# Kernel optimization log

Measured on AMD Instinct MI355X. Metric: run time of the kernel, lower is better.

Reference implementation:

```python
import jax, jax.numpy as jnp
import numpy as np

BN_EPS = 1e-5

def _conv1x1(h, w, b):
    # h: [N, Cin, L], w: [Cout, Cin], b: [Cout] -> [N, Cout, L]
    return jnp.einsum('ncl,oc->nol', h, w) + b[None, :, None]

def _bn_eval(h, g, bt, m, v):
    return (h - m[None, :, None]) / jnp.sqrt(v[None, :, None] + BN_EPS) * g[None, :, None] + bt[None, :, None]

def setup_inputs() -> dict:
    key = jax.random.key(0)
    ks = jax.random.split(key, 20)
    B, R, L, F = 1024, 16, 12, 16
    num_cat, num_cont, V, D = 8, 8, 1000, 32
    FD = F * D  # 512
    H1, H2 = 64, 32
    s = 0.05
    idx_part = jax.random.randint(ks[0], (B, R, L, num_cat), 0, V).astype(jnp.float32)
    cont_part = jax.random.normal(ks[1], (B, R, L, num_cont), dtype=jnp.float32)
    x = jnp.concatenate([idx_part, cont_part], axis=-1)
    return {
        'x': x,
        'cat_emb': jax.random.normal(ks[2], (num_cat, V, D), dtype=jnp.float32) * s,
        'cat_lin': jax.random.normal(ks[3], (num_cat, V, D), dtype=jnp.float32) * s,
        'cont_w': jax.random.normal(ks[4], (num_cont, D), dtype=jnp.float32) * s,
        'cont_b': jax.random.normal(ks[5], (num_cont, D), dtype=jnp.float32) * s,
        'cont_lin_w': jax.random.normal(ks[6], (num_cont, D), dtype=jnp.float32) * s,
        'cont_lin_b': jax.random.normal(ks[7], (num_cont, D), dtype=jnp.float32) * s,
        'fin_bias': jnp.zeros((D,), dtype=jnp.float32),
        'dnn1_w': jax.random.normal(ks[8], (H1, FD), dtype=jnp.float32) * s,
        'dnn1_b': jnp.zeros((H1,), dtype=jnp.float32),
        'bn1_g': jnp.ones((H1,), dtype=jnp.float32),
        'bn1_bt': jnp.zeros((H1,), dtype=jnp.float32),
        'bn1_m': jnp.zeros((H1,), dtype=jnp.float32),
        'bn1_v': jnp.ones((H1,), dtype=jnp.float32),
        'dnn2_w': jax.random.normal(ks[9], (H2, H1), dtype=jnp.float32) * s,
        'dnn2_b': jnp.zeros((H2,), dtype=jnp.float32),
        'bn2_g': jnp.ones((H2,), dtype=jnp.float32),
        'bn2_bt': jnp.zeros((H2,), dtype=jnp.float32),
        'bn2_m': jnp.zeros((H2,), dtype=jnp.float32),
        'bn2_v': jnp.ones((H2,), dtype=jnp.float32),
        'out_w': jax.random.normal(ks[10], (D, H2), dtype=jnp.float32) * s,
        'out_b': jnp.zeros((D,), dtype=jnp.float32),
    }

def reference(x, cat_emb, cat_lin, cont_w, cont_b, cont_lin_w, cont_lin_b, fin_bias,
              dnn1_w, dnn1_b, bn1_g, bn1_bt, bn1_m, bn1_v,
              dnn2_w, dnn2_b, bn2_g, bn2_bt, bn2_m, bn2_v,
              out_w, out_b):
    B, R, L, F = x.shape
    N = B * R
    num_cat = cat_emb.shape[0]
    D = cat_emb.shape[2]
    xf = x.reshape(N, L, F)
    idx = xf[:, :, :num_cat].astype(jnp.int32)   # [N, L, C]
    cont = xf[:, :, num_cat:]                    # [N, L, J]
    f_ids = jnp.arange(num_cat)[None, None, :]   # broadcast field ids
    # embedding path -> [N, D, field, L]
    cat_e = cat_emb[f_ids, idx].transpose(0, 3, 2, 1)                                   # [N,D,C,L]
    cont_e = (cont[..., None] * cont_w[None, None] + cont_b[None, None]).transpose(0, 3, 2, 1)  # [N,D,J,L]
    emb_all = jnp.concatenate([cat_e, cont_e], axis=2)                                  # [N,D,F,L]
    # FM second-order interaction
    ssum = emb_all.sum(axis=2)
    fm = 0.5 * (ssum * ssum - (emb_all * emb_all).sum(axis=2))                          # [N,D,L]
    # linear terms
    cat_l = cat_lin[f_ids, idx].transpose(0, 3, 2, 1)
    cont_l = (cont[..., None] * cont_lin_w[None, None] + cont_lin_b[None, None]).transpose(0, 3, 2, 1)
    linear_terms = cat_l.sum(axis=2) + cont_l.sum(axis=2) + fin_bias[None, :, None]     # [N,D,L]
    # DNN over field-major concatenated channels [N, F*D, L]
    dnn_in = emb_all.transpose(0, 2, 1, 3).reshape(N, F * D, L)
    h = jax.nn.relu(_bn_eval(_conv1x1(dnn_in, dnn1_w, dnn1_b), bn1_g, bn1_bt, bn1_m, bn1_v))
    h = jax.nn.relu(_bn_eval(_conv1x1(h, dnn2_w, dnn2_b), bn2_g, bn2_bt, bn2_m, bn2_v))
    dnn_out = _conv1x1(h, out_w, out_b)                                                 # [N,D,L]
    out = linear_terms + fm + dnn_out
    return out.transpose(0, 2, 1)  # [N, L, D]
```

## Files before the change

kernel.cpp:

```cpp
#include <hip/hip_runtime.h>
#include <hip/hip_bf16.h>

typedef __attribute__((ext_vector_type(8))) short short8;
typedef __attribute__((ext_vector_type(4))) float f32x4;
typedef __attribute__((ext_vector_type(4))) unsigned short ushort4n;

#define BLK 256
#define NTILES 6144

#define A1_OFF   0
#define FMC_OFF  0
#define A2_OFF   8448
#define A3_OFF   12544
#define PART_OFF 18432
#define XS_OFF   26624
#define SMEM_BYTES 28672

#define WS_B1F  0
#define WS_B2F  256
#define WS_W1F  512
#define WS_W2F  37888
#define WS_W3F  41984
#define WS_WFM  44032
#define WS_EL   49152

__global__ void prep_kernel(
    const float* __restrict__ w1, const float* __restrict__ b1,
    const float* __restrict__ g1, const float* __restrict__ bt1,
    const float* __restrict__ m1, const float* __restrict__ v1,
    const float* __restrict__ w2, const float* __restrict__ b2,
    const float* __restrict__ g2, const float* __restrict__ bt2,
    const float* __restrict__ m2, const float* __restrict__ v2,
    const float* __restrict__ w3,
    const float* __restrict__ cat_emb, const float* __restrict__ cat_lin,
    const float* __restrict__ cont_w,  const float* __restrict__ cont_b,
    const float* __restrict__ cont_lw, const float* __restrict__ cont_lb,
    const float* __restrict__ fin_bias,
    float* __restrict__ bias1f, float* __restrict__ bias2f,
    __hip_bfloat16* __restrict__ W1f, __hip_bfloat16* __restrict__ W2f,
    __hip_bfloat16* __restrict__ W3f, __hip_bfloat16* __restrict__ WFMf,
    unsigned* __restrict__ ELb)
{
    int t  = blockIdx.x * blockDim.x + threadIdx.x;
    int nt = gridDim.x * blockDim.x;
    if (t < 64) {
        float s = g1[t] / sqrtf(v1[t] + 1e-5f);
        float cbsum = 0.f;
        for (int f = 0; f < 8; ++f)
            for (int d = 0; d < 32; ++d)
                cbsum += w1[t * 512 + 256 + f * 32 + d] * cont_b[f * 32 + d];
        bias1f[t] = (b1[t] + cbsum - m1[t]) * s + bt1[t];
    }
    if (t >= 64 && t < 96) {
        int o = t - 64;
        float s = g2[o] / sqrtf(v2[o] + 1e-5f);
        bias2f[o] = (b2[o] - m2[o]) * s + bt2[o];
    }
    for (int i = t; i < 8 * 1000 * 32; i += nt) {
        __hip_bfloat16 eb = __float2bfloat16(cat_emb[i]);
        __hip_bfloat16 lb = __float2bfloat16(cat_lin[i]);
        unsigned eu = *(unsigned short*)&eb;
        unsigned lu = *(unsigned short*)&lb;
        ELb[i] = eu | (lu << 16);
    }
    for (int fi = t; fi < 4 * 9 * 512; fi += nt) {
        int j = fi & 7, lane = (fi >> 3) & 63, t2 = fi >> 9;
        int kk = t2 % 9, ct = t2 / 9;
        int k = kk * 32 + ((lane >> 4) << 3) + j;
        int n = ct * 16 + (lane & 15);
        float s = g1[n] / sqrtf(v1[n] + 1e-5f);
        float val = 0.f;
        if (k < 256) val = s * w1[n * 512 + k];
        else if (k < 264) {
            int f = k - 256; float a = 0.f;
            for (int d = 0; d < 32; ++d)
                a += w1[n * 512 + 256 + f * 32 + d] * cont_w[f * 32 + d];
            val = s * a;
        }
        W1f[fi] = __float2bfloat16(val);
    }
    for (int fi = t; fi < 2048; fi += nt) {
        int j = fi & 7, lane = (fi >> 3) & 63, fmct = fi >> 9;
        int kl = ((lane >> 4) << 3) + j;
        int col = fmct * 16 + (lane & 15);
        int d = col & 31, s = col >> 5;
        float val = 0.f;
        if (s == 0) {
            if (kl < 8) val = cont_w[kl * 32 + d];
            else if (kl == 16) { float a = 0.f; for (int f = 0; f < 8; ++f) a += cont_b[f * 32 + d]; val = a; }
        } else {
            if (kl < 8) val = cont_lw[kl * 32 + d] - cont_w[kl * 32 + d] * cont_b[kl * 32 + d];
            else if (kl < 16) { float w = cont_w[(kl - 8) * 32 + d]; val = -0.5f * w * w; }
            else if (kl == 16) {
                float a = fin_bias[d];
                for (int f = 0; f < 8; ++f)
                    a += cont_lb[f * 32 + d] - 0.5f * cont_b[f * 32 + d] * cont_b[f * 32 + d];
                val = a;
            }
        }
        WFMf[fi] = __float2bfloat16(val);
    }
    for (int fi = t; fi < 2048; fi += nt) {
        int j = fi & 7, lane = (fi >> 3) & 63, kt = fi >> 9;
        int ct = kt >> 1, kk = kt & 1;
        int k = kk * 32 + ((lane >> 4) << 3) + j;
        int n = ct * 16 + (lane & 15);
        float s = g2[n] / sqrtf(v2[n] + 1e-5f);
        W2f[fi] = __float2bfloat16(s * w2[n * 64 + k]);
    }
    for (int fi = t; fi < 1024; fi += nt) {
        int j = fi & 7, lane = (fi >> 3) & 63, ct = fi >> 9;
        int k = ((lane >> 4) << 3) + j;
        int n = ct * 16 + (lane & 15);
        W3f[fi] = __float2bfloat16(w3[n * 32 + k]);
    }
}

static __device__ __forceinline__ unsigned short bf16bits(float f) {
    __hip_bfloat16 h = __float2bfloat16(f);
    return *(unsigned short*)&h;
}

__global__ __launch_bounds__(BLK, 5) void fused_kernel(
    const float* __restrict__ x,
    const float* __restrict__ bias1f, const float* __restrict__ bias2f,
    const float* __restrict__ out_b,
    const __hip_bfloat16* __restrict__ W1f,
    const __hip_bfloat16* __restrict__ W2f,
    const __hip_bfloat16* __restrict__ W3f,
    const __hip_bfloat16* __restrict__ WFMf,
    const unsigned* __restrict__ ELb,
    float* __restrict__ out)
{
    __shared__ __align__(16) char smem[SMEM_BYTES];
    const int tid  = threadIdx.x;
    const int lane = tid & 63;
    const int wv   = tid >> 6;
    const int tile = blockIdx.x;
    const int rt2 = wv >> 1, ct2 = wv & 1;

    if (tid < 128)
        ((float4*)(smem + XS_OFF))[tid] = ((const float4*)(x + (size_t)tile * 512))[tid];
    __syncthreads();

    {
        const int p = tid >> 3, d0 = (tid & 7) << 2, g = d0 >> 3, rtp = p >> 4;
        const float* xs = (const float*)(smem + XS_OFF) + p * 16;
        float4 xi0 = ((const float4*)xs)[0];
        float4 xi1 = ((const float4*)xs)[1];
        float4 xc0 = ((const float4*)xs)[2];
        float4 xc1 = ((const float4*)xs)[3];
        float idxf[8] = {xi0.x, xi0.y, xi0.z, xi0.w, xi1.x, xi1.y, xi1.z, xi1.w};
        float cf[8]   = {xc0.x, xc0.y, xc0.z, xc0.w, xc1.x, xc1.y, xc1.z, xc1.w};

        float4 ssum = {0.f, 0.f, 0.f, 0.f};
        float4 lin  = {0.f, 0.f, 0.f, 0.f};
        float4 ssq  = {0.f, 0.f, 0.f, 0.f};

        char* aw = smem + A1_OFF + rtp * 1024 + ((p & 15) + 16 * g) * 16 + (d0 & 7) * 2;
        #pragma unroll
        for (int f = 0; f < 8; ++f) {
            int ix = (int)idxf[f];
            uint4 v = *(const uint4*)(ELb + ((f * 1000 + ix) * 32 + d0));
            float e0 = __uint_as_float(v.x << 16), l0 = __uint_as_float(v.x & 0xFFFF0000u);
            float e1 = __uint_as_float(v.y << 16), l1 = __uint_as_float(v.y & 0xFFFF0000u);
            float e2 = __uint_as_float(v.z << 16), l2 = __uint_as_float(v.z & 0xFFFF0000u);
            float e3 = __uint_as_float(v.w << 16), l3 = __uint_as_float(v.w & 0xFFFF0000u);
            ssum.x += e0; ssum.y += e1; ssum.z += e2; ssum.w += e3;
            ssq.x = fmaf(e0, e0, ssq.x); ssq.y = fmaf(e1, e1, ssq.y);
            ssq.z = fmaf(e2, e2, ssq.z); ssq.w = fmaf(e3, e3, ssq.w);
            lin.x += l0; lin.y += l1; lin.z += l2; lin.w += l3;
            ushort4n ev = {(unsigned short)v.x, (unsigned short)v.y,
                           (unsigned short)v.z, (unsigned short)v.w};
            *(ushort4n*)(aw + f * 2048) = ev;
        }
        {
            char* c8 = smem + A1_OFF + 8 * 2048 + rtp * 1024 + ((p & 15) + 16 * g) * 16;
            ushort4n lo = {0, 0, 0, 0}, hi = {0, 0, 0, 0};
            if (g == 0) {
                lo = (ushort4n){bf16bits(cf[0]), bf16bits(cf[1]), bf16bits(cf[2]), bf16bits(cf[3])};
                hi = (ushort4n){bf16bits(cf[4]), bf16bits(cf[5]), bf16bits(cf[6]), bf16bits(cf[7])};
            } else if (g == 1) {
                lo = (ushort4n){bf16bits(cf[0]*cf[0]), bf16bits(cf[1]*cf[1]), bf16bits(cf[2]*cf[2]), bf16bits(cf[3]*cf[3])};
                hi = (ushort4n){bf16bits(cf[4]*cf[4]), bf16bits(cf[5]*cf[5]), bf16bits(cf[6]*cf[6]), bf16bits(cf[7]*cf[7])};
            } else if (g == 2) {
                lo = (ushort4n){0x3F80, 0, 0, 0};
            }
            *(ushort4n*)c8 = lo;
            *(ushort4n*)(c8 + 8) = hi;
        }
        float4 G;
        G.x = lin.x - 0.5f * ssq.x; G.y = lin.y - 0.5f * ssq.y;
        G.z = lin.z - 0.5f * ssq.z; G.w = lin.w - 0.5f * ssq.w;
        float4 o0 = {ssum.x, G.x, ssum.y, G.y};
        float4 o1 = {ssum.z, G.z, ssum.w, G.w};
        *(float4*)(smem + PART_OFF + (p * 32 + d0) * 8)      = o0;
        *(float4*)(smem + PART_OFF + (p * 32 + d0) * 8 + 16) = o1;
    }
    __syncthreads();

    const short8* W1v  = (const short8*)W1f;
    const short8* WFMv = (const short8*)WFMf;
    f32x4 ah0 = {0,0,0,0}, ah1 = {0,0,0,0};
    f32x4 fm0 = {0,0,0,0}, fm1 = {0,0,0,0};
    #pragma unroll
    for (int kk = 0; kk < 9; ++kk) {
        short8 b  = W1v[(wv * 9 + kk) * 64 + lane];
        short8 a0 = *(const short8*)(smem + A1_OFF + kk * 2048 + lane * 16);
        short8 a1 = *(const short8*)(smem + A1_OFF + kk * 2048 + 1024 + lane * 16);
        ah0 = __builtin_amdgcn_mfma_f32_16x16x32_bf16(a0, b, ah0, 0, 0, 0);
        ah1 = __builtin_amdgcn_mfma_f32_16x16x32_bf16(a1, b, ah1, 0, 0, 0);
        if (kk == 8) {
            short8 bfm = WFMv[wv * 64 + lane];
            fm0 = __builtin_amdgcn_mfma_f32_16x16x32_bf16(a0, bfm, fm0, 0, 0, 0);
            fm1 = __builtin_amdgcn_mfma_f32_16x16x32_bf16(a1, bfm, fm1, 0, 0, 0);
        }
    }
    __syncthreads();

    {
        const float bo1 = bias1f[wv * 16 + (lane & 15)];
        const int coll = (wv * 16 + (lane & 15)) & 31;
        const int kk2 = wv >> 1;
        const int nsub = coll >> 3;
        const int jof = (coll & 7) * 2;
        const int rbase = (lane >> 4) << 2;
        #pragma unroll
        for (int rt = 0; rt < 2; ++rt) {
            f32x4 acc = rt ? ah1 : ah0;
            #pragma unroll
            for (int r = 0; r < 4; ++r) {
                float h = fmaxf(acc[r] + bo1, 0.f);
                *(__hip_bfloat16*)(smem + A2_OFF + (kk2 * 2 + rt) * 1024 + ((rbase + r) + 16 * nsub) * 16 + jof)
                    = __float2bfloat16(h);
            }
        }
        const int colf = wv * 16 + (lane & 15);
        const int d = colf & 31, s = colf >> 5;
        #pragma unroll
        for (int rt = 0; rt < 2; ++rt) {
            f32x4 acc = rt ? fm1 : fm0;
            #pragma unroll
            for (int r = 0; r < 4; ++r) {
                int row = rt * 16 + rbase + r;
                *(float*)(smem + FMC_OFF + (row * 66 + d * 2 + s) * 4) = acc[r];
            }
        }
    }
    __syncthreads();

    const short8* W2v = (const short8*)W2f;
    f32x4 acc2 = {0,0,0,0};
    {
        short8 b0 = W2v[(ct2 * 2 + 0) * 64 + lane];
        short8 b1 = W2v[(ct2 * 2 + 1) * 64 + lane];
        short8 a0 = *(const short8*)(smem + A2_OFF + (0 * 2 + rt2) * 1024 + lane * 16);
        acc2 = __builtin_amdgcn_mfma_f32_16x16x32_bf16(a0, b0, acc2, 0, 0, 0);
        short8 a1 = *(const short8*)(smem + A2_OFF + (1 * 2 + rt2) * 1024 + lane * 16);
        acc2 = __builtin_amdgcn_mfma_f32_16x16x32_bf16(a1, b1, acc2, 0, 0, 0);
    }
    {
        const float bo2 = bias2f[ct2 * 16 + (lane & 15)];
        const int col2 = ct2 * 16 + (lane & 15);
        const int nsub2 = col2 >> 3;
        const int jof = (col2 & 7) * 2;
        const int rbase = (lane >> 4) << 2;
        #pragma unroll
        for (int r = 0; r < 4; ++r) {
            float h = fmaxf(acc2[r] + bo2, 0.f);
            *(__hip_bfloat16*)(smem + A3_OFF + rt2 * 1024 + ((rbase + r) + 16 * nsub2) * 16 + jof)
                = __float2bfloat16(h);
        }
    }
    __syncthreads();

    {
        const short8* W3v = (const short8*)W3f;
        short8 b3 = W3v[ct2 * 64 + lane];
        short8 a3 = *(const short8*)(smem + A3_OFF + rt2 * 1024 + lane * 16);
        f32x4 z = {0,0,0,0};
        f32x4 acc3 = __builtin_amdgcn_mfma_f32_16x16x32_bf16(a3, b3, z, 0, 0, 0);

        const int dcol = ct2 * 16 + (lane & 15);
        const float ob = out_b[dcol];
        const int rbase = (lane >> 4) << 2;
        size_t outbase = (size_t)tile * 1024;
        #pragma unroll
        for (int r = 0; r < 4; ++r) {
            int p = rt2 * 16 + rbase + r;
            float2 sg = *(const float2*)(smem + FMC_OFF + (p * 66 + dcol * 2) * 4);
            float2 pc = *(const float2*)(smem + PART_OFF + (p * 32 + dcol) * 8);
            float S = pc.x + sg.x;
            out[outbase + p * 32 + dcol] = acc3[r] + ob + pc.y + sg.y + 0.5f * S * S;
        }
    }
}

extern "C" void kernel_launch(void* const* d_in, const int* in_sizes, int n_in,
                              void* d_out, int out_size, void* d_ws, size_t ws_size,
                              hipStream_t stream) {
    const float* x        = (const float*)d_in[0];
    const float* cat_emb  = (const float*)d_in[1];
    const float* cat_lin  = (const float*)d_in[2];
    const float* cont_w   = (const float*)d_in[3];
    const float* cont_b   = (const float*)d_in[4];
    const float* cont_lw  = (const float*)d_in[5];
    const float* cont_lb  = (const float*)d_in[6];
    const float* fin_bias = (const float*)d_in[7];
    const float* dnn1_w   = (const float*)d_in[8];
    const float* dnn1_b   = (const float*)d_in[9];
    const float* bn1_g    = (const float*)d_in[10];
    const float* bn1_bt   = (const float*)d_in[11];
    const float* bn1_m    = (const float*)d_in[12];
    const float* bn1_v    = (const float*)d_in[13];
    const float* dnn2_w   = (const float*)d_in[14];
    const float* dnn2_b   = (const float*)d_in[15];
    const float* bn2_g    = (const float*)d_in[16];
    const float* bn2_bt   = (const float*)d_in[17];
    const float* bn2_m    = (const float*)d_in[18];
    const float* bn2_v    = (const float*)d_in[19];
    const float* out_w    = (const float*)d_in[20];
    const float* out_b    = (const float*)d_in[21];

    char* ws = (char*)d_ws;
    float* bias1f = (float*)(ws + WS_B1F);
    float* bias2f = (float*)(ws + WS_B2F);
    __hip_bfloat16* W1f  = (__hip_bfloat16*)(ws + WS_W1F);
    __hip_bfloat16* W2f  = (__hip_bfloat16*)(ws + WS_W2F);
    __hip_bfloat16* W3f  = (__hip_bfloat16*)(ws + WS_W3F);
    __hip_bfloat16* WFMf = (__hip_bfloat16*)(ws + WS_WFM);
    unsigned* ELb = (unsigned*)(ws + WS_EL);

    hipLaunchKernelGGL(prep_kernel, dim3(256), dim3(BLK), 0, stream,
                       dnn1_w, dnn1_b, bn1_g, bn1_bt, bn1_m, bn1_v,
                       dnn2_w, dnn2_b, bn2_g, bn2_bt, bn2_m, bn2_v,
                       out_w, cat_emb, cat_lin, cont_w, cont_b, cont_lw, cont_lb,
                       fin_bias, bias1f, bias2f, W1f, W2f, W3f, WFMf, ELb);

    hipLaunchKernelGGL(fused_kernel, dim3(NTILES), dim3(BLK), 0, stream,
                       x, bias1f, bias2f, out_b, W1f, W2f, W3f, WFMf, ELb,
                       (float*)d_out);
}
```

Baseline: 40.97 us.

## Double tile to 64 positions per 512-thread block and fold FM results into partials

Each block now handles 64 positions with 8 waves instead of 32 with 4, halving the grid and re-laying out shared-memory A1/A2 tiles with four row-tiles per k-slice. The FM MFMA outputs are added directly into the per-position partial buffer instead of going to a separate FM scratch region, which removes one shared buffer and simplifies the epilogue. The larger block costs more shared memory per block (57KB) and lowers launch bounds occupancy to 4. Each W1 fragment is still loaded per wave, but two row-tile waves now share each column tile within a block.

```diff
diff --git a/kernel.cpp b/kernel.cpp
--- a/kernel.cpp
+++ b/kernel.cpp
@@ -5,16 +5,16 @@
 typedef __attribute__((ext_vector_type(4))) float f32x4;
 typedef __attribute__((ext_vector_type(4))) unsigned short ushort4n;
 
-#define BLK 256
-#define NTILES 6144
+#define BLK 512
+#define MT 64
+#define NTILES 3072
 
 #define A1_OFF   0
-#define FMC_OFF  0
-#define A2_OFF   8448
-#define A3_OFF   12544
-#define PART_OFF 18432
-#define XS_OFF   26624
-#define SMEM_BYTES 28672
+#define A2_OFF   0
+#define A3_OFF   8192
+#define PART_OFF 36864
+#define XS_OFF   53248
+#define SMEM_BYTES 57344
 
 #define WS_B1F  0
 #define WS_B2F  256
@@ -121,7 +121,7 @@
     return *(unsigned short*)&h;
 }
 
-__global__ __launch_bounds__(BLK, 5) void fused_kernel(
+__global__ __launch_bounds__(BLK, 4) void fused_kernel(
     const float* __restrict__ x,
     const float* __restrict__ bias1f, const float* __restrict__ bias2f,
     const float* __restrict__ out_b,
@@ -137,10 +137,9 @@
     const int lane = tid & 63;
     const int wv   = tid >> 6;
     const int tile = blockIdx.x;
-    const int rt2 = wv >> 1, ct2 = wv & 1;
-
-    if (tid < 128)
-        ((float4*)(smem + XS_OFF))[tid] = ((const float4*)(x + (size_t)tile * 512))[tid];
+
+    if (tid < 256)
+        ((float4*)(smem + XS_OFF))[tid] = ((const float4*)(x + (size_t)tile * 1024))[tid];
     __syncthreads();
 
     {
@@ -172,10 +171,10 @@
             lin.x += l0; lin.y += l1; lin.z += l2; lin.w += l3;
             ushort4n ev = {(unsigned short)v.x, (unsigned short)v.y,
                            (unsigned short)v.z, (unsigned short)v.w};
-            *(ushort4n*)(aw + f * 2048) = ev;
+            *(ushort4n*)(aw + f * 4096) = ev;
         }
         {
-            char* c8 = smem + A1_OFF + 8 * 2048 + rtp * 1024 + ((p & 15) + 16 * g) * 16;
+            char* c8 = smem + A1_OFF + (8 * 4 + rtp) * 1024 + ((p & 15) + 16 * g) * 16;
             ushort4n lo = {0, 0, 0, 0}, hi = {0, 0, 0, 0};
             if (g == 0) {
                 lo = (ushort4n){bf16bits(cf[0]), bf16bits(cf[1]), bf16bits(cf[2]), bf16bits(cf[3])};
@@ -201,17 +200,19 @@
 
     const short8* W1v  = (const short8*)W1f;
     const short8* WFMv = (const short8*)WFMf;
+    const int ct1 = wv & 3, rth = wv >> 2;
+    const int rt0 = rth * 2, rt1 = rth * 2 + 1;
     f32x4 ah0 = {0,0,0,0}, ah1 = {0,0,0,0};
     f32x4 fm0 = {0,0,0,0}, fm1 = {0,0,0,0};
     #pragma unroll
     for (int kk = 0; kk < 9; ++kk) {
-        short8 b  = W1v[(wv * 9 + kk) * 64 + lane];
-        short8 a0 = *(const short8*)(smem + A1_OFF + kk * 2048 + lane * 16);
-        short8 a1 = *(const short8*)(smem + A1_OFF + kk * 2048 + 1024 + lane * 16);
+        short8 b  = W1v[(ct1 * 9 + kk) * 64 + lane];
+        short8 a0 = *(const short8*)(smem + A1_OFF + (kk * 4 + rt0) * 1024 + lane * 16);
+        short8 a1 = *(const short8*)(smem + A1_OFF + (kk * 4 + rt1) * 1024 + lane * 16);
         ah0 = __builtin_amdgcn_mfma_f32_16x16x32_bf16(a0, b, ah0, 0, 0, 0);
         ah1 = __builtin_amdgcn_mfma_f32_16x16x32_bf16(a1, b, ah1, 0, 0, 0);
         if (kk == 8) {
-            short8 bfm = WFMv[wv * 64 + lane];
+            short8 bfm = WFMv[ct1 * 64 + lane];
             fm0 = __builtin_amdgcn_mfma_f32_16x16x32_bf16(a0, bfm, fm0, 0, 0, 0);
             fm1 = __builtin_amdgcn_mfma_f32_16x16x32_bf16(a1, bfm, fm1, 0, 0, 0);
         }
@@ -219,44 +220,49 @@
     __syncthreads();
 
     {
-        const float bo1 = bias1f[wv * 16 + (lane & 15)];
-        const int coll = (wv * 16 + (lane & 15)) & 31;
-        const int kk2 = wv >> 1;
+        const float bo1 = bias1f[ct1 * 16 + (lane & 15)];
+        const int colh = ct1 * 16 + (lane & 15);
+        const int kk2 = colh >> 5;
+        const int coll = colh & 31;
         const int nsub = coll >> 3;
         const int jof = (coll & 7) * 2;
         const int rbase = (lane >> 4) << 2;
         #pragma unroll
-        for (int rt = 0; rt < 2; ++rt) {
-            f32x4 acc = rt ? ah1 : ah0;
+        for (int h = 0; h < 2; ++h) {
+            f32x4 acc = h ? ah1 : ah0;
+            const int rt = h ? rt1 : rt0;
             #pragma unroll
             for (int r = 0; r < 4; ++r) {
-                float h = fmaxf(acc[r] + bo1, 0.f);
-                *(__hip_bfloat16*)(smem + A2_OFF + (kk2 * 2 + rt) * 1024 + ((rbase + r) + 16 * nsub) * 16 + jof)
-                    = __float2bfloat16(h);
+                float hv = fmaxf(acc[r] + bo1, 0.f);
+                *(__hip_bfloat16*)(smem + A2_OFF + (kk2 * 4 + rt) * 1024 + ((rbase + r) + 16 * nsub) * 16 + jof)
+                    = __float2bfloat16(hv);
             }
         }
-        const int colf = wv * 16 + (lane & 15);
+        const int colf = ct1 * 16 + (lane & 15);
         const int d = colf & 31, s = colf >> 5;
         #pragma unroll
-        for (int rt = 0; rt < 2; ++rt) {
-            f32x4 acc = rt ? fm1 : fm0;
+        for (int h = 0; h < 2; ++h) {
+            f32x4 acc = h ? fm1 : fm0;
+            const int rt = h ? rt1 : rt0;
             #pragma unroll
             for (int r = 0; r < 4; ++r) {
-                int row = rt * 16 + rbase + r;
-                *(float*)(smem + FMC_OFF + (row * 66 + d * 2 + s) * 4) = acc[r];
+                int p = rt * 16 + rbase + r;
+                float* slot = (float*)(smem + PART_OFF + (p * 32 + d) * 8 + s * 4);
+                *slot += acc[r];
             }
         }
     }
     __syncthreads();
 
+    const int rt2 = wv >> 1, ct2 = wv & 1;
     const short8* W2v = (const short8*)W2f;
     f32x4 acc2 = {0,0,0,0};
     {
         short8 b0 = W2v[(ct2 * 2 + 0) * 64 + lane];
         short8 b1 = W2v[(ct2 * 2 + 1) * 64 + lane];
-        short8 a0 = *(const short8*)(smem + A2_OFF + (0 * 2 + rt2) * 1024 + lane * 16);
+        short8 a0 = *(const short8*)(smem + A2_OFF + (0 * 4 + rt2) * 1024 + lane * 16);
         acc2 = __builtin_amdgcn_mfma_f32_16x16x32_bf16(a0, b0, acc2, 0, 0, 0);
-        short8 a1 = *(const short8*)(smem + A2_OFF + (1 * 2 + rt2) * 1024 + lane * 16);
+        short8 a1 = *(const short8*)(smem + A2_OFF + (1 * 4 + rt2) * 1024 + lane * 16);
         acc2 = __builtin_amdgcn_mfma_f32_16x16x32_bf16(a1, b1, acc2, 0, 0, 0);
     }
     {
@@ -275,23 +281,22 @@
     __syncthreads();
 
     {
+        const int rt3 = wv >> 1, ct3 = wv & 1;
         const short8* W3v = (const short8*)W3f;
-        short8 b3 = W3v[ct2 * 64 + lane];
-        short8 a3 = *(const short8*)(smem + A3_OFF + rt2 * 1024 + lane * 16);
+        short8 b3 = W3v[ct3 * 64 + lane];
+        short8 a3 = *(const short8*)(smem + A3_OFF + rt3 * 1024 + lane * 16);
         f32x4 z = {0,0,0,0};
         f32x4 acc3 = __builtin_amdgcn_mfma_f32_16x16x32_bf16(a3, b3, z, 0, 0, 0);
 
-        const int dcol = ct2 * 16 + (lane & 15);
+        const int dcol = ct3 * 16 + (lane & 15);
         const float ob = out_b[dcol];
         const int rbase = (lane >> 4) << 2;
-        size_t outbase = (size_t)tile * 1024;
+        size_t outbase = (size_t)tile * (MT * 32);
         #pragma unroll
         for (int r = 0; r < 4; ++r) {
-            int p = rt2 * 16 + rbase + r;
-            float2 sg = *(const float2*)(smem + FMC_OFF + (p * 66 + dcol * 2) * 4);
-            float2 pc = *(const float2*)(smem + PART_OFF + (p * 32 + dcol) * 8);
-            float S = pc.x + sg.x;
-            out[outbase + p * 32 + dcol] = acc3[r] + ob + pc.y + sg.y + 0.5f * S * S;
+            int p = rt3 * 16 + rbase + r;
+            float2 sg = *(const float2*)(smem + PART_OFF + (p * 32 + dcol) * 8);
+            out[outbase + p * 32 + dcol] = acc3[r] + ob + sg.y + 0.5f * sg.x * sg.x;
         }
     }
 }
@@ -331,7 +336,7 @@
     __hip_bfloat16* WFMf = (__hip_bfloat16*)(ws + WS_WFM);
     unsigned* ELb = (unsigned*)(ws + WS_EL);
 
-    hipLaunchKernelGGL(prep_kernel, dim3(256), dim3(BLK), 0, stream,
+    hipLaunchKernelGGL(prep_kernel, dim3(256), dim3(256), 0, stream,
                        dnn1_w, dnn1_b, bn1_g, bn1_bt, bn1_m, bn1_v,
                        dnn2_w, dnn2_b, bn2_g, bn2_bt, bn2_m, bn2_v,
                        out_w, cat_emb, cat_lin, cont_w, cont_b, cont_lw, cont_lb,
```

Result: slower. 46.30 us (+13.0%).

## Remove barriers by giving each wave private layer-2/3 work and separate smem regions

Applied to the files above, without the earlier changes.

Moves the A2/A3 scratch regions so they no longer alias A1, which lets the barrier after the first MFMA loop be removed. The FM results are now accumulated in place into the PART slots instead of a separate FMC buffer. Each wave now computes both layer-2 column tiles for its own row tile and writes layer-3 input to a private chunk, which drops another block-wide barrier. The cost is more LDS per block (may reduce occupancy with 5 blocks per CU) and duplicated layer-2 MFMAs across waves. The in-place += on PART relies on the later s=0/s=1 writers being distinct, and they are.

```diff
diff --git a/kernel.cpp b/kernel.cpp
--- a/kernel.cpp
+++ b/kernel.cpp
@@ -9,12 +9,11 @@
 #define NTILES 6144
 
 #define A1_OFF   0
-#define FMC_OFF  0
-#define A2_OFF   8448
-#define A3_OFF   12544
-#define PART_OFF 18432
-#define XS_OFF   26624
-#define SMEM_BYTES 28672
+#define A3_OFF   0
+#define A2_OFF   18432
+#define PART_OFF 22528
+#define XS_OFF   30720
+#define SMEM_BYTES 32768
 
 #define WS_B1F  0
 #define WS_B2F  256
@@ -137,7 +136,6 @@
     const int lane = tid & 63;
     const int wv   = tid >> 6;
     const int tile = blockIdx.x;
-    const int rt2 = wv >> 1, ct2 = wv & 1;
 
     if (tid < 128)
         ((float4*)(smem + XS_OFF))[tid] = ((const float4*)(x + (size_t)tile * 512))[tid];
@@ -216,82 +214,82 @@
             fm1 = __builtin_amdgcn_mfma_f32_16x16x32_bf16(a1, bfm, fm1, 0, 0, 0);
         }
     }
-    __syncthreads();
 
     {
         const float bo1 = bias1f[wv * 16 + (lane & 15)];
-        const int coll = (wv * 16 + (lane & 15)) & 31;
-        const int kk2 = wv >> 1;
+        const int colh = wv * 16 + (lane & 15);
+        const int kk2 = colh >> 5;
+        const int coll = colh & 31;
         const int nsub = coll >> 3;
         const int jof = (coll & 7) * 2;
         const int rbase = (lane >> 4) << 2;
         #pragma unroll
-        for (int rt = 0; rt < 2; ++rt) {
-            f32x4 acc = rt ? ah1 : ah0;
+        for (int h = 0; h < 2; ++h) {
+            f32x4 acc = h ? ah1 : ah0;
             #pragma unroll
             for (int r = 0; r < 4; ++r) {
-                float h = fmaxf(acc[r] + bo1, 0.f);
-                *(__hip_bfloat16*)(smem + A2_OFF + (kk2 * 2 + rt) * 1024 + ((rbase + r) + 16 * nsub) * 16 + jof)
-                    = __float2bfloat16(h);
+                float hv = fmaxf(acc[r] + bo1, 0.f);
+                *(__hip_bfloat16*)(smem + A2_OFF + (kk2 * 2 + h) * 1024 + ((rbase + r) + 16 * nsub) * 16 + jof)
+                    = __float2bfloat16(hv);
             }
         }
         const int colf = wv * 16 + (lane & 15);
         const int d = colf & 31, s = colf >> 5;
         #pragma unroll
-        for (int rt = 0; rt < 2; ++rt) {
-            f32x4 acc = rt ? fm1 : fm0;
+        for (int h = 0; h < 2; ++h) {
+            f32x4 acc = h ? fm1 : fm0;
             #pragma unroll
             for (int r = 0; r < 4; ++r) {
-                int row = rt * 16 + rbase + r;
-                *(float*)(smem + FMC_OFF + (row * 66 + d * 2 + s) * 4) = acc[r];
+                int p = h * 16 + rbase + r;
+                float* slot = (float*)(smem + PART_OFF + (p * 32 + d) * 8 + s * 4);
+                *slot += acc[r];
             }
         }
     }
     __syncthreads();
 
-    const short8* W2v = (const short8*)W2f;
-    f32x4 acc2 = {0,0,0,0};
     {
-        short8 b0 = W2v[(ct2 * 2 + 0) * 64 + lane];
-        short8 b1 = W2v[(ct2 * 2 + 1) * 64 + lane];
-        short8 a0 = *(const short8*)(smem + A2_OFF + (0 * 2 + rt2) * 1024 + lane * 16);
-        acc2 = __builtin_amdgcn_mfma_f32_16x16x32_bf16(a0, b0, acc2, 0, 0, 0);
-        short8 a1 = *(const short8*)(smem + A2_OFF + (1 * 2 + rt2) * 1024 + lane * 16);
-        acc2 = __builtin_amdgcn_mfma_f32_16x16x32_bf16(a1, b1, acc2, 0, 0, 0);
-    }
-    {
-        const float bo2 = bias2f[ct2 * 16 + (lane & 15)];
-        const int col2 = ct2 * 16 + (lane & 15);
-        const int nsub2 = col2 >> 3;
-        const int jof = (col2 & 7) * 2;
-        const int rbase = (lane >> 4) << 2;
-        #pragma unroll
-        for (int r = 0; r < 4; ++r) {
-            float h = fmaxf(acc2[r] + bo2, 0.f);
-            *(__hip_bfloat16*)(smem + A3_OFF + rt2 * 1024 + ((rbase + r) + 16 * nsub2) * 16 + jof)
-                = __float2bfloat16(h);
-        }
-    }
-    __syncthreads();
-
-    {
+        const int rt = wv & 1, ct3 = wv >> 1;
+        const short8* W2v = (const short8*)W2f;
+        short8 a20 = *(const short8*)(smem + A2_OFF + (0 * 2 + rt) * 1024 + lane * 16);
+        short8 a21 = *(const short8*)(smem + A2_OFF + (1 * 2 + rt) * 1024 + lane * 16);
+        f32x4 acc2c0 = {0,0,0,0}, acc2c1 = {0,0,0,0};
+        acc2c0 = __builtin_amdgcn_mfma_f32_16x16x32_bf16(a20, W2v[(0 * 2 + 0) * 64 + lane], acc2c0, 0, 0, 0);
+        acc2c0 = __builtin_amdgcn_mfma_f32_16x16x32_bf16(a21, W2v[(0 * 2 + 1) * 64 + lane], acc2c0, 0, 0, 0);
+        acc2c1 = __builtin_amdgcn_mfma_f32_16x16x32_bf16(a20, W2v[(1 * 2 + 0) * 64 + lane], acc2c1, 0, 0, 0);
+        acc2c1 = __builtin_amdgcn_mfma_f32_16x16x32_bf16(a21, W2v[(1 * 2 + 1) * 64 + lane], acc2c1, 0, 0, 0);
+
+        char* mychunk = smem + A3_OFF + wv * 1024;
+        {
+            const int rbase = (lane >> 4) << 2;
+            #pragma unroll
+            for (int c = 0; c < 2; ++c) {
+                f32x4 acc = c ? acc2c1 : acc2c0;
+                const float bo2 = bias2f[c * 16 + (lane & 15)];
+                const int k = c * 16 + (lane & 15);
+                const int nsub = k >> 3, jof = (k & 7) * 2;
+                #pragma unroll
+                for (int r = 0; r < 4; ++r) {
+                    float h = fmaxf(acc[r] + bo2, 0.f);
+                    *(__hip_bfloat16*)(mychunk + ((nsub * 16 + (rbase + r)) * 16 + jof))
+                        = __float2bfloat16(h);
+                }
+            }
+        }
+        short8 a3 = *(const short8*)(mychunk + lane * 16);
         const short8* W3v = (const short8*)W3f;
-        short8 b3 = W3v[ct2 * 64 + lane];
-        short8 a3 = *(const short8*)(smem + A3_OFF + rt2 * 1024 + lane * 16);
         f32x4 z = {0,0,0,0};
-        f32x4 acc3 = __builtin_amdgcn_mfma_f32_16x16x32_bf16(a3, b3, z, 0, 0, 0);
-
-        const int dcol = ct2 * 16 + (lane & 15);
+        f32x4 acc3 = __builtin_amdgcn_mfma_f32_16x16x32_bf16(a3, W3v[ct3 * 64 + lane], z, 0, 0, 0);
+
+        const int dcol = ct3 * 16 + (lane & 15);
         const float ob = out_b[dcol];
         const int rbase = (lane >> 4) << 2;
         size_t outbase = (size_t)tile * 1024;
         #pragma unroll
         for (int r = 0; r < 4; ++r) {
-            int p = rt2 * 16 + rbase + r;
-            float2 sg = *(const float2*)(smem + FMC_OFF + (p * 66 + dcol * 2) * 4);
-            float2 pc = *(const float2*)(smem + PART_OFF + (p * 32 + dcol) * 8);
-            float S = pc.x + sg.x;
-            out[outbase + p * 32 + dcol] = acc3[r] + ob + pc.y + sg.y + 0.5f * S * S;
+            int p = rt * 16 + rbase + r;
+            float2 sg = *(const float2*)(smem + PART_OFF + (p * 32 + dcol) * 8);
+            out[outbase + p * 32 + dcol] = acc3[r] + ob + sg.y + 0.5f * sg.x * sg.x;
         }
     }
 }
@@ -331,7 +329,7 @@
     __hip_bfloat16* WFMf = (__hip_bfloat16*)(ws + WS_WFM);
     unsigned* ELb = (unsigned*)(ws + WS_EL);
 
-    hipLaunchKernelGGL(prep_kernel, dim3(256), dim3(BLK), 0, stream,
+    hipLaunchKernelGGL(prep_kernel, dim3(256), dim3(256), 0, stream,
                        dnn1_w, dnn1_b, bn1_g, bn1_bt, bn1_m, bn1_v,
                        dnn2_w, dnn2_b, bn2_g, bn2_bt, bn2_m, bn2_v,
                        out_w, cat_emb, cat_lin, cont_w, cont_b, cont_lw, cont_lb,
```

Measured after the change: 42.89 us. 1.05x slower.
